# Optimization experiments

Hardware: AMD Instinct MI355X
Metric: run time of the kernel (lower is better)

## Reference

```python
import jax, jax.numpy as jnp
import numpy as np
from jax import lax

T, B, C_IN, C_OUT, H, W = 8, 16, 64, 64, 64, 64
TAU = 2.0
V_TH = 1.0
V_RESET = 0.0


def setup_inputs() -> dict:
    key = jax.random.key(0)
    k1, k2 = jax.random.split(key)
    x = jax.random.normal(k1, (T, B, C_IN, H, W), dtype=jnp.float32)
    # Kaiming-ish scale for a 3x3 conv
    conv_w = jax.random.normal(k2, (C_OUT, C_IN, 3, 3), dtype=jnp.float32) * (2.0 / (C_IN * 9)) ** 0.5
    return {"x": x, "conv_w": conv_w}


def _conv2d_same(x, w):
    # x: [N, C_in, H, W], w: [C_out, C_in, 3, 3], padding=1, no bias
    return lax.conv_general_dilated(
        x, w, window_strides=(1, 1), padding=((1, 1), (1, 1)),
        dimension_numbers=("NCHW", "OIHW", "NCHW"))


def _lif_scan(z):
    # z: [T, B, C, H, W]; leaky integrate-and-fire with hard reset
    def step(v, x_t):
        v = v + (x_t - (v - V_RESET)) / TAU
        spike = (v >= V_TH).astype(v.dtype)
        v = v * (1.0 - spike) + V_RESET * spike
        return v, spike
    v0 = jnp.zeros(z.shape[1:], dtype=z.dtype)
    _, spikes = lax.scan(step, v0, z)
    return spikes  # [T, B, C, H, W]


def reference(x, conv_w):
    # x: [T, B, C_in, H, W]
    z = _conv2d_same(x.reshape(T * B, C_IN, H, W), conv_w)
    z = z.reshape(T, B, C_OUT, H, W)
    return _lif_scan(z)
```

## Files before the change

kernel.cpp:

```cpp
#include <hip/hip_runtime.h>


#define T_STEPS 8
#define BATCH   16
#define CIN     64
#define COUT    64
#define IMH     64
#define IMW     64
#define HW      (IMH * IMW)
#define X_ELEMS (T_STEPS * BATCH * CIN * HW)
#define W_ELEMS (COUT * CIN * 9)

__global__ void transpose_weights(const float* __restrict__ wf, float* __restrict__ wt) {
    int i = blockIdx.x * 256 + threadIdx.x;
    if (i < W_ELEMS) {
        int co = i / 576;
        int g  = i - co * 576;
        wt[g * 64 + co] = wf[i];
    }
}

__device__ __forceinline__ float stage_load(const float* xim, int h0, int w0,
                                            int q) {
    int ci  = q / 100;
    int rem = q - ci * 100;
    int hh  = rem / 10;
    int wl  = rem - hh * 10;
    int gh  = h0 - 1 + hh;
    int gw  = w0 - 1 + wl;
    float val = 0.0f;
    if ((unsigned)gh < IMH && (unsigned)gw < IMW)
        val = xim[ci * HW + gh * IMW + gw];
    return val;
}

__global__ __launch_bounds__(256, 4)
void snn_conv_lif_f0(const float* __restrict__ x, const float* __restrict__ wt,
                     float* __restrict__ out) {
    __shared__ float xt[CIN][10][12];

    const int tid  = threadIdx.x;
    const int lane = tid & 63;
    const int wid  = __builtin_amdgcn_readfirstlane(tid >> 6);

    const int b    = blockIdx.x >> 6;
    const int tile = blockIdx.x & 63;
    const int h0   = (tile >> 3) << 3;
    const int w0   = (tile & 7) << 3;
    const int ph   = lane >> 3;
    const int pw   = lane & 7;
    const int cobase = wid << 4;
    const int oh = h0 + ph, ow = w0 + pw;

    double v[16];
#pragma unroll
    for (int i = 0; i < 16; ++i) v[i] = 0.0;

    float r[25];
    {
        const float* xim = x + (size_t)b * CIN * HW;
#pragma unroll
        for (int j = 0; j < 25; ++j)
            r[j] = stage_load(xim, h0, w0, tid + j * 256);
    }

    for (int t = 0; t < T_STEPS; ++t) {
        __syncthreads();
#pragma unroll
        for (int j = 0; j < 25; ++j) {
            int q   = tid + j * 256;
            int ci  = q / 100;
            int rem = q - ci * 100;
            int hh  = rem / 10;
            int wl  = rem - hh * 10;
            xt[ci][hh][wl] = r[j];
        }
        __syncthreads();

        if (t + 1 < T_STEPS) {
            const float* xim = x + (size_t)((t + 1) * BATCH + b) * CIN * HW;
#pragma unroll
            for (int j = 0; j < 25; ++j)
                r[j] = stage_load(xim, h0, w0, tid + j * 256);
        }

        float z[16];
#pragma unroll
        for (int i = 0; i < 16; ++i) z[i] = 0.0f;

        for (int ci = 0; ci < CIN; ++ci) {
            float nb[9];
#pragma unroll
            for (int dy = 0; dy < 3; ++dy)
#pragma unroll
                for (int dx = 0; dx < 3; ++dx)
                    nb[dy * 3 + dx] = xt[ci][ph + dy][pw + dx];

#pragma unroll
            for (int k = 0; k < 9; ++k) {
                float xv = nb[k];
                const float4* w4 = (const float4*)(wt + (ci * 9 + k) * 64 + cobase);
                float4 wa = w4[0], wb = w4[1], wc = w4[2], wd = w4[3];
                z[0]  = __builtin_fmaf(wa.x, xv, z[0]);
                z[1]  = __builtin_fmaf(wa.y, xv, z[1]);
                z[2]  = __builtin_fmaf(wa.z, xv, z[2]);
                z[3]  = __builtin_fmaf(wa.w, xv, z[3]);
                z[4]  = __builtin_fmaf(wb.x, xv, z[4]);
                z[5]  = __builtin_fmaf(wb.y, xv, z[5]);
                z[6]  = __builtin_fmaf(wb.z, xv, z[6]);
                z[7]  = __builtin_fmaf(wb.w, xv, z[7]);
                z[8]  = __builtin_fmaf(wc.x, xv, z[8]);
                z[9]  = __builtin_fmaf(wc.y, xv, z[9]);
                z[10] = __builtin_fmaf(wc.z, xv, z[10]);
                z[11] = __builtin_fmaf(wc.w, xv, z[11]);
                z[12] = __builtin_fmaf(wd.x, xv, z[12]);
                z[13] = __builtin_fmaf(wd.y, xv, z[13]);
                z[14] = __builtin_fmaf(wd.z, xv, z[14]);
                z[15] = __builtin_fmaf(wd.w, xv, z[15]);
            }
        }

        size_t obase = ((size_t)(t * BATCH + b) * COUT + cobase) * HW
                     + (size_t)oh * IMW + ow;
#pragma unroll
        for (int i = 0; i < 16; ++i) {
            double d  = (double)z[i] - v[i];
            double nv = v[i] + d * 0.5;
            bool  sp  = (nv >= 1.0);
            out[obase + (size_t)i * HW] = sp ? 1.0f : 0.0f;
            v[i] = sp ? 0.0 : nv;
        }
    }
}

__global__ __launch_bounds__(256)
void snn_conv_lif_f0_direct(const float* __restrict__ x, const float* __restrict__ cw,
                            float* __restrict__ out) {
    __shared__ float xt[CIN][10][12];

    const int tid  = threadIdx.x;
    const int lane = tid & 63;
    const int wid  = __builtin_amdgcn_readfirstlane(tid >> 6);
    const int b    = blockIdx.x >> 6;
    const int tile = blockIdx.x & 63;
    const int h0   = (tile >> 3) << 3;
    const int w0   = (tile & 7) << 3;
    const int ph   = lane >> 3, pw = lane & 7;
    const int cobase = wid << 4;
    const int oh = h0 + ph, ow = w0 + pw;

    double v[16];
#pragma unroll
    for (int i = 0; i < 16; ++i) v[i] = 0.0;

    for (int t = 0; t < T_STEPS; ++t) {
        __syncthreads();
        const float* xim = x + (size_t)(t * BATCH + b) * CIN * HW;
#pragma unroll
        for (int j = 0; j < 25; ++j) {
            int q   = tid + j * 256;
            int ci  = q / 100;
            int rem = q - ci * 100;
            int hh  = rem / 10;
            int wl  = rem - hh * 10;
            xt[ci][hh][wl] = stage_load(xim, h0, w0, q);
        }
        __syncthreads();

        float z[16];
#pragma unroll
        for (int i = 0; i < 16; ++i) z[i] = 0.0f;

        for (int ci = 0; ci < CIN; ++ci) {
            float nb[9];
#pragma unroll
            for (int dy = 0; dy < 3; ++dy)
#pragma unroll
                for (int dx = 0; dx < 3; ++dx)
                    nb[dy * 3 + dx] = xt[ci][ph + dy][pw + dx];
            const float* wp = cw + ci * 9;
#pragma unroll
            for (int k = 0; k < 9; ++k) {
                float xv = nb[k];
#pragma unroll
                for (int i = 0; i < 16; ++i)
                    z[i] = __builtin_fmaf(wp[(cobase + i) * (CIN * 9) + k], xv, z[i]);
            }
        }

        size_t obase = ((size_t)(t * BATCH + b) * COUT + cobase) * HW
                     + (size_t)oh * IMW + ow;
#pragma unroll
        for (int i = 0; i < 16; ++i) {
            double d  = (double)z[i] - v[i];
            double nv = v[i] + d * 0.5;
            bool  sp  = (nv >= 1.0);
            out[obase + (size_t)i * HW] = sp ? 1.0f : 0.0f;
            v[i] = sp ? 0.0 : nv;
        }
    }
}

extern "C" void kernel_launch(void* const* d_in, const int* in_sizes, int n_in,
                              void* d_out, int out_size, void* d_ws, size_t ws_size,
                              hipStream_t stream) {
    const float* x  = (const float*)d_in[0];
    const float* wf = (const float*)d_in[1];
    if (n_in >= 2) {
        if (in_sizes[0] == W_ELEMS || in_sizes[1] == X_ELEMS) {
            x  = (const float*)d_in[1];
            wf = (const float*)d_in[0];
        }
    }
    float* out = (float*)d_out;
    (void)out_size;

    dim3 grid(BATCH * 64);
    dim3 block(256);

    if (ws_size >= (size_t)W_ELEMS * sizeof(float)) {
        float* wt = (float*)d_ws;
        hipLaunchKernelGGL(transpose_weights, dim3((W_ELEMS + 255) / 256), block, 0, stream, wf, wt);
        hipLaunchKernelGGL(snn_conv_lif_f0, grid, block, 0, stream, x, wt, out);
    } else {
        hipLaunchKernelGGL(snn_conv_lif_f0_direct, grid, block, 0, stream, x, wf, out);
    }
}
```

Before: 527.4 us.

## Stage input tiles via async global-to-LDS loads with double-buffered shared memory

Replaces the register-staged prefetch of the next timestep's input halo with direct global-to-LDS loads (global_load_lds) into a second LDS buffer. Each timestep now needs one barrier instead of two, and the 25 prefetch registers are freed. Out-of-bounds halo elements are loaded from a zeroed scratch area in the workspace, which is cleared with a memset. In exchange, LDS use per block roughly doubles, which can limit how many blocks fit on a CU. Correctness also relies on the async loads having completed before the barrier, and nothing in the code explicitly waits for that.

```diff
diff --git a/kernel.cpp b/kernel.cpp
--- a/kernel.cpp
+++ b/kernel.cpp
@@ -10,6 +10,10 @@
 #define HW      (IMH * IMW)
 #define X_ELEMS (T_STEPS * BATCH * CIN * HW)
 #define W_ELEMS (COUT * CIN * 9)
+#define W_BYTES (W_ELEMS * 4)
+
+typedef const __attribute__((address_space(1))) float gfloat;
+typedef __attribute__((address_space(3))) float lfloat;
 
 __global__ void transpose_weights(const float* __restrict__ wf, float* __restrict__ wt) {
     int i = blockIdx.x * 256 + threadIdx.x;
@@ -20,24 +24,29 @@
     }
 }
 
-__device__ __forceinline__ float stage_load(const float* xim, int h0, int w0,
-                                            int q) {
-    int ci  = q / 100;
-    int rem = q - ci * 100;
-    int hh  = rem / 10;
-    int wl  = rem - hh * 10;
-    int gh  = h0 - 1 + hh;
-    int gw  = w0 - 1 + wl;
-    float val = 0.0f;
-    if ((unsigned)gh < IMH && (unsigned)gw < IMW)
-        val = xim[ci * HW + gh * IMW + gw];
-    return val;
+__device__ __forceinline__ void stage_async(const float* __restrict__ xim,
+                                            float* lds_lin,
+                                            const float* __restrict__ zp,
+                                            int h0, int w0, int tid) {
+#pragma unroll
+    for (int j = 0; j < 25; ++j) {
+        int q   = tid + j * 256;
+        int ci  = q / 100;
+        int rem = q - ci * 100;
+        int hh  = rem / 10;
+        int wl  = rem - hh * 10;
+        int gh  = h0 - 1 + hh;
+        int gw  = w0 - 1 + wl;
+        const float* src = ((unsigned)gh < IMH && (unsigned)gw < IMW)
+                         ? (xim + ci * HW + gh * IMW + gw) : zp;
+        __builtin_amdgcn_global_load_lds((gfloat*)src, (lfloat*)(lds_lin + q), 4, 0, 0);
+    }
 }
 
 __global__ __launch_bounds__(256, 4)
 void snn_conv_lif_f0(const float* __restrict__ x, const float* __restrict__ wt,
-                     float* __restrict__ out) {
-    __shared__ float xt[CIN][10][12];
+                     const float* __restrict__ zp, float* __restrict__ out) {
+    __shared__ float xt[2][6400];
 
     const int tid  = threadIdx.x;
     const int lane = tid & 63;
@@ -56,34 +65,17 @@
 #pragma unroll
     for (int i = 0; i < 16; ++i) v[i] = 0.0;
 
-    float r[25];
-    {
-        const float* xim = x + (size_t)b * CIN * HW;
-#pragma unroll
-        for (int j = 0; j < 25; ++j)
-            r[j] = stage_load(xim, h0, w0, tid + j * 256);
-    }
+    stage_async(x + (size_t)b * CIN * HW, xt[0], zp, h0, w0, tid);
+    int cur = 0;
 
     for (int t = 0; t < T_STEPS; ++t) {
         __syncthreads();
-#pragma unroll
-        for (int j = 0; j < 25; ++j) {
-            int q   = tid + j * 256;
-            int ci  = q / 100;
-            int rem = q - ci * 100;
-            int hh  = rem / 10;
-            int wl  = rem - hh * 10;
-            xt[ci][hh][wl] = r[j];
-        }
-        __syncthreads();
-
-        if (t + 1 < T_STEPS) {
-            const float* xim = x + (size_t)((t + 1) * BATCH + b) * CIN * HW;
-#pragma unroll
-            for (int j = 0; j < 25; ++j)
-                r[j] = stage_load(xim, h0, w0, tid + j * 256);
-        }
-
+
+        if (t + 1 < T_STEPS)
+            stage_async(x + (size_t)((t + 1) * BATCH + b) * CIN * HW,
+                        xt[cur ^ 1], zp, h0, w0, tid);
+
+        const float* xb = xt[cur];
         float z[16];
 #pragma unroll
         for (int i = 0; i < 16; ++i) z[i] = 0.0f;
@@ -94,7 +86,7 @@
             for (int dy = 0; dy < 3; ++dy)
 #pragma unroll
                 for (int dx = 0; dx < 3; ++dx)
-                    nb[dy * 3 + dx] = xt[ci][ph + dy][pw + dx];
+                    nb[dy * 3 + dx] = xb[ci * 100 + (ph + dy) * 10 + (pw + dx)];
 
 #pragma unroll
             for (int k = 0; k < 9; ++k) {
@@ -130,6 +122,7 @@
             out[obase + (size_t)i * HW] = sp ? 1.0f : 0.0f;
             v[i] = sp ? 0.0 : nv;
         }
+        cur ^= 1;
     }
 }
 
@@ -163,7 +156,12 @@
             int rem = q - ci * 100;
             int hh  = rem / 10;
             int wl  = rem - hh * 10;
-            xt[ci][hh][wl] = stage_load(xim, h0, w0, q);
+            int gh  = h0 - 1 + hh;
+            int gw  = w0 - 1 + wl;
+            float val = 0.0f;
+            if ((unsigned)gh < IMH && (unsigned)gw < IMW)
+                val = xim[ci * HW + gh * IMW + gw];
+            xt[ci][hh][wl] = val;
         }
         __syncthreads();
 
@@ -215,14 +213,13 @@
     float* out = (float*)d_out;
     (void)out_size;
 
-    dim3 grid(BATCH * 64);
-    dim3 block(256);
-
-    if (ws_size >= (size_t)W_ELEMS * sizeof(float)) {
+    if (ws_size >= (size_t)W_BYTES + 1024) {
         float* wt = (float*)d_ws;
-        hipLaunchKernelGGL(transpose_weights, dim3((W_ELEMS + 255) / 256), block, 0, stream, wf, wt);
-        hipLaunchKernelGGL(snn_conv_lif_f0, grid, block, 0, stream, x, wt, out);
+        float* zp = (float*)((char*)d_ws + W_BYTES);
+        hipMemsetAsync(zp, 0, 1024, stream);
+        hipLaunchKernelGGL(transpose_weights, dim3((W_ELEMS + 255) / 256), dim3(256), 0, stream, wf, wt);
+        hipLaunchKernelGGL(snn_conv_lif_f0, dim3(BATCH * 64), dim3(256), 0, stream, x, wt, zp, out);
     } else {
-        hipLaunchKernelGGL(snn_conv_lif_f0_direct, grid, block, 0, stream, x, wf, out);
-    }
-}
+        hipLaunchKernelGGL(snn_conv_lif_f0_direct, dim3(BATCH * 64), dim3(256), 0, stream, x, wf, out);
+    }
+}
```

Measured after the change: 699.6 us. 32.7% more time.
